# Kernel tuning notes

Hardware: AMD Instinct MI355X
Metric: run time of the kernel (lower is better)

## Reference

```python
import jax, jax.numpy as jnp
import numpy as np

O, I, K, N = 32, 32, 13, 4096  # out feats, in feats, kernel taps, lattice sites


def setup_inputs() -> dict:
    key = jax.random.key(0)
    k1, k2, k3, k4 = jax.random.split(key, 4)
    x = jax.random.normal(k1, (I, N), dtype=jnp.float32)
    Wconv = jax.random.normal(k2, (O, I, K), dtype=jnp.float32) * 0.1
    bconv = jnp.zeros((O,), dtype=jnp.float32)
    mask = (jax.random.uniform(k3, (N, O, I, K)) > 0.1).astype(jnp.float32)
    shifts = jax.random.randint(k4, (N, K), 0, N, dtype=jnp.int32)
    return {"x": x, "Wconv": Wconv, "bconv": bconv, "mask": mask, "shifts": shifts}


def reference(x, Wconv, bconv, mask, shifts):
    # gather input columns for every site's stencil: (I, N, K)
    g = x[:, shifts]
    # per-site masked weight contraction, vectorized over sites n
    # y[o, n] = sum_{i,k} Wconv[o,i,k] * mask[n,o,i,k] * x[i, shifts[n,k]]
    y = jnp.einsum('oik,noik,ink->on', Wconv, mask, g)
    y = y + bconv[:, None]
    e = float(np.e)
    scale = (2.0 + 2.0 * e) / (e - 1.0)
    return (jax.nn.sigmoid(y) - 0.5) * scale
```

## Files before the change

### kernel.cpp

```cpp
#include <hip/hip_runtime.h>
#include <math.h>

#define O_  32
#define I_  32
#define K_  13
#define N_  4096
#define IK  (I_ * K_)
#define OIK (O_ * IK)
#define NB  4

typedef float f32x4 __attribute__((ext_vector_type(4)));

__global__ __launch_bounds__(256, 4) void plaq_kernel(
    const float* __restrict__ x,
    const float* __restrict__ W,
    const float* __restrict__ b,
    const float* __restrict__ mask,
    const int*   __restrict__ shifts,
    float* __restrict__ out)
{
    __shared__ __align__(16) float g_lds[NB][IK];
    const int n0  = blockIdx.x * NB;
    const int tid = threadIdx.x;

    for (int idx = tid; idx < NB * IK; idx += 256) {
        int nl = idx / IK;
        int r  = idx - nl * IK;
        int i  = r / K_;
        int k  = r - i * K_;
        int s  = shifts[(n0 + nl) * K_ + k];
        g_lds[nl][r] = x[i * N_ + s];
    }

    const int o  = tid >> 3;
    const int s8 = tid & 7;
    const f32x4* w4 = (const f32x4*)(W + o * IK);
    f32x4 w[13];
#pragma unroll
    for (int m = 0; m < 13; ++m) w[m] = w4[s8 + 8 * m];
    const float bo = b[o];

    __syncthreads();

    const float scale = (float)((2.0 + 2.0 * M_E) / (M_E - 1.0));

    for (int nl = 0; nl < NB; ++nl) {
        const int n = n0 + nl;
        const f32x4* m4 = (const f32x4*)(mask + (size_t)n * OIK + o * IK);
        const f32x4* g4 = (const f32x4*)(&g_lds[nl][0]);

        float a0 = 0.f, a1 = 0.f, a2 = 0.f, a3 = 0.f;
#pragma unroll
        for (int m = 0; m < 13; ++m) {
            f32x4 mv = __builtin_nontemporal_load(&m4[s8 + 8 * m]);
            f32x4 wg = w[m] * g4[s8 + 8 * m];
            a0 = fmaf(mv.x, wg.x, a0);
            a1 = fmaf(mv.y, wg.y, a1);
            a2 = fmaf(mv.z, wg.z, a2);
            a3 = fmaf(mv.w, wg.w, a3);
        }
        float acc = (a0 + a1) + (a2 + a3);

        acc += __shfl_down(acc, 4);
        acc += __shfl_down(acc, 2);
        acc += __shfl_down(acc, 1);

        if (s8 == 0) {
            float y  = acc + bo;
            float sg = 1.0f / (1.0f + __expf(-y));
            out[o * N_ + n] = (sg - 0.5f) * scale;
        }
    }
}

extern "C" void kernel_launch(void* const* d_in, const int* in_sizes, int n_in,
                              void* d_out, int out_size, void* d_ws, size_t ws_size,
                              hipStream_t stream) {
    const float* x      = (const float*)d_in[0];
    const float* Wconv  = (const float*)d_in[1];
    const float* bconv  = (const float*)d_in[2];
    const float* mask   = (const float*)d_in[3];
    const int*   shifts = (const int*)d_in[4];
    float* out = (float*)d_out;

    plaq_kernel<<<N_ / NB, 256, 0, stream>>>(x, Wconv, bconv, mask, shifts, out);
}
```

Before: 291.5 us.

## Coalesce mask loads with flat thread mapping and LDS reduction

```diff
diff --git a/kernel.cpp b/kernel.cpp
--- a/kernel.cpp
+++ b/kernel.cpp
@@ -8,6 +8,8 @@
 #define IK  (I_ * K_)
 #define OIK (O_ * IK)
 #define NB  4
+#define NF4 (OIK / 4)
+#define CPO (IK / 4)
 
 typedef float f32x4 __attribute__((ext_vector_type(4)));
 
@@ -20,6 +22,7 @@
     float* __restrict__ out)
 {
     __shared__ __align__(16) float g_lds[NB][IK];
+    __shared__ __align__(16) float red[NF4];
     const int n0  = blockIdx.x * NB;
     const int tid = threadIdx.x;
 
@@ -32,44 +35,52 @@
         g_lds[nl][r] = x[i * N_ + s];
     }
 
-    const int o  = tid >> 3;
-    const int s8 = tid & 7;
-    const f32x4* w4 = (const f32x4*)(W + o * IK);
-    f32x4 w[13];
+    const f32x4* W4 = (const f32x4*)W;
+    f32x4 w13[13];
 #pragma unroll
-    for (int m = 0; m < 13; ++m) w[m] = w4[s8 + 8 * m];
-    const float bo = b[o];
+    for (int j = 0; j < 13; ++j) w13[j] = W4[j * 256 + tid];
+    const float bo = b[tid >> 3];
 
     __syncthreads();
 
     const float scale = (float)((2.0 + 2.0 * M_E) / (M_E - 1.0));
+    const int r4_0 = tid - (tid / CPO) * CPO;
 
     for (int nl = 0; nl < NB; ++nl) {
         const int n = n0 + nl;
-        const f32x4* m4 = (const f32x4*)(mask + (size_t)n * OIK + o * IK);
-        const f32x4* g4 = (const f32x4*)(&g_lds[nl][0]);
+        const f32x4* m4 = (const f32x4*)(mask + (size_t)n * OIK);
+        const float* g  = &g_lds[nl][0];
 
-        float a0 = 0.f, a1 = 0.f, a2 = 0.f, a3 = 0.f;
+        int r4 = r4_0;
 #pragma unroll
-        for (int m = 0; m < 13; ++m) {
-            f32x4 mv = __builtin_nontemporal_load(&m4[s8 + 8 * m]);
-            f32x4 wg = w[m] * g4[s8 + 8 * m];
-            a0 = fmaf(mv.x, wg.x, a0);
-            a1 = fmaf(mv.y, wg.y, a1);
-            a2 = fmaf(mv.z, wg.z, a2);
-            a3 = fmaf(mv.w, wg.w, a3);
+        for (int j = 0; j < 13; ++j) {
+            f32x4 mv = m4[j * 256 + tid];
+            f32x4 gv = *(const f32x4*)(g + 4 * r4);
+            f32x4 wg = w13[j] * gv;
+            float p  = fmaf(mv.w, wg.w,
+                       fmaf(mv.z, wg.z,
+                       fmaf(mv.y, wg.y, mv.x * wg.x)));
+            red[j * 256 + tid] = p;
+            r4 += 48; if (r4 >= CPO) r4 -= CPO;
         }
-        float acc = (a0 + a1) + (a2 + a3);
+        __syncthreads();
 
-        acc += __shfl_down(acc, 4);
-        acc += __shfl_down(acc, 2);
-        acc += __shfl_down(acc, 1);
-
-        if (s8 == 0) {
-            float y  = acc + bo;
-            float sg = 1.0f / (1.0f + __expf(-y));
-            out[o * N_ + n] = (sg - 0.5f) * scale;
+        {
+            const int o = tid >> 3, s = tid & 7;
+            const float* c = &red[CPO * o + 13 * s];
+            float v = c[0];
+#pragma unroll
+            for (int q = 1; q < 13; ++q) v += c[q];
+            v += __shfl_down(v, 4);
+            v += __shfl_down(v, 2);
+            v += __shfl_down(v, 1);
+            if (s == 0) {
+                float y  = v + bo;
+                float sg = 1.0f / (1.0f + __expf(-y));
+                out[o * N_ + n] = (sg - 0.5f) * scale;
+            }
         }
+        __syncthreads();
     }
 }
 
```

Result: slower. 313.6 us (+7.6%).
